# Optimization experiments

Hardware: AMD Instinct MI355X
Metric: run time of the kernel (lower is better)

## Reference

```python
import jax, jax.numpy as jnp
import numpy as np

GROUPS = 32
EPS = 1e-6


def group_norm(x, gamma, beta):
    # x: [b, c, h, w], normalize over (c//GROUPS, h, w) within each group
    b, c, h, w = x.shape
    xg = x.reshape(b, GROUPS, c // GROUPS, h, w)
    mu = xg.mean(axis=(2, 3, 4), keepdims=True)
    var = xg.var(axis=(2, 3, 4), keepdims=True)
    xn = ((xg - mu) * jax.lax.rsqrt(var + EPS)).reshape(b, c, h, w)
    return xn * gamma[None, :, None, None] + beta[None, :, None, None]


def conv1x1(x, W, b):
    # 1x1 conv == channel GEMM. W: [out_c, in_c]
    return jnp.einsum('bchw,oc->bohw', x, W) + b[None, :, None, None]


def setup_inputs() -> dict:
    key = jax.random.key(0)
    ks = jax.random.split(key, 4)
    B, C, H, W = 4, 512, 64, 64
    wscale = 0.02
    return {
        'x': jax.random.normal(ks[0], (B, C, H, W), dtype=jnp.float32),
        'gn_w': jnp.ones((C,), dtype=jnp.float32),
        'gn_b': jnp.zeros((C,), dtype=jnp.float32),
        'q_w': jax.random.normal(ks[1], (C, C), dtype=jnp.float32) * wscale,
        'q_b': jnp.zeros((C,), dtype=jnp.float32),
        'k_w': jax.random.normal(ks[2], (C, C), dtype=jnp.float32) * wscale,
        'k_b': jnp.zeros((C,), dtype=jnp.float32),
        'v_w': jax.random.normal(ks[3], (C, C), dtype=jnp.float32) * wscale,
        'v_b': jnp.zeros((C,), dtype=jnp.float32),
    }


def reference(x, gn_w, gn_b, q_w, q_b, k_w, k_b, v_w, v_b):
    h_ = group_norm(x, gn_w, gn_b)
    q = conv1x1(h_, q_w, q_b)
    k = conv1x1(h_, k_w, k_b)
    v = conv1x1(h_, v_w, v_b)
    b, c, h, w = q.shape
    hw = h * w
    qf = q.reshape(b, c, hw)
    kf = k.reshape(b, c, hw)
    vf = v.reshape(b, c, hw)
    # attn[b, i, j] = sum_c q[b, c, i] * k[b, c, j] / sqrt(c)
    attn = jnp.einsum('bci,bcj->bij', qf, kf) * (c ** -0.5)
    attn = jax.nn.softmax(attn, axis=2)
    # A[b, c, i] = sum_j v[b, c, j] * attn[b, i, j]  (== bmm(v, attn^T))
    A = jnp.einsum('bcj,bij->bci', vf, attn).reshape(b, c, h, w)
    return x + A
```

## Files before the change

kernel.cpp:

```cpp
#include <hip/hip_runtime.h>
#include <hip/hip_bf16.h>

typedef __hip_bfloat16 bf16;
typedef __attribute__((ext_vector_type(8))) short short8;
typedef __attribute__((ext_vector_type(4))) float f32x4;
typedef __attribute__((ext_vector_type(8))) unsigned short u16x8;
typedef __attribute__((ext_vector_type(4))) unsigned short u16x4;

#define HWSZ 4096
#define CH 512
#define BATCH 4
#define NGROUPS 32
#define CPG 16
#define PER ((size_t)CH * HWSZ)

#define GLL16(gp, lp)                                                         \
  __builtin_amdgcn_global_load_lds(                                           \
      (const __attribute__((address_space(1))) void*)(gp),                    \
      (__attribute__((address_space(3))) void*)(lp), 16, 0, 0)

__device__ __forceinline__ float b2f(bf16 v) { return __bfloat162float(v); }
__device__ __forceinline__ bf16 f2b(float v) { return __float2bfloat16(v); }

__global__ void gn_part_kernel(const float* __restrict__ x, float2* __restrict__ gpart) {
  int bg = blockIdx.x >> 3, chunk = blockIdx.x & 7;
  size_t base = (size_t)bg * (CPG * HWSZ) + (size_t)chunk * 8192;
  int tid = threadIdx.x;
  float s = 0.f, ss = 0.f;
  const float4* xp = (const float4*)(x + base);
#pragma unroll
  for (int it = 0; it < 8; ++it) {
    float4 v = xp[tid + it * 256];
    s += v.x + v.y + v.z + v.w;
    ss += v.x * v.x + v.y * v.y + v.z * v.z + v.w * v.w;
  }
  __shared__ float rs[256], rss[256];
  rs[tid] = s; rss[tid] = ss;
  __syncthreads();
  for (int off = 128; off > 0; off >>= 1) {
    if (tid < off) { rs[tid] += rs[tid + off]; rss[tid] += rss[tid + off]; }
    __syncthreads();
  }
  if (tid == 0) gpart[blockIdx.x] = make_float2(rs[0], rss[0]);
}

__global__ void gn_final_kernel(const float2* __restrict__ gpart,
                                const float* __restrict__ gw, const float* __restrict__ gb,
                                float* __restrict__ sca, float* __restrict__ shf) {
  int idx = blockIdx.x * 256 + threadIdx.x;
  int b = idx >> 9, c = idx & 511;
  int bg = b * NGROUPS + (c >> 4);
  float s = 0.f, ss = 0.f;
#pragma unroll
  for (int t = 0; t < 8; ++t) {
    float2 p = gpart[bg * 8 + t];
    s += p.x; ss += p.y;
  }
  const float N = (float)(CPG * HWSZ);
  float mu = s / N;
  float var = ss / N - mu * mu;
  float inv = rsqrtf(var + 1e-6f);
  float a = inv * gw[c];
  sca[idx] = a;
  shf[idx] = gb[c] - mu * a;
}

__global__ void wconv_kernel(const float* __restrict__ qw, const float* __restrict__ kw,
                             const float* __restrict__ vw,
                             bf16* __restrict__ wq, bf16* __restrict__ wk, bf16* __restrict__ wv) {
  int i = blockIdx.x * 256 + threadIdx.x;
  wq[i] = f2b(qw[i]);
  wk[i] = f2b(kw[i]);
  wv[i] = f2b(vw[i]);
}

__global__ void h_apply_kernel(const float* __restrict__ x, const float* __restrict__ sca,
                               const float* __restrict__ shf, bf16* __restrict__ hT, int b0) {
  int p0 = blockIdx.x * 64, c0 = blockIdx.y * 64;
  int b = b0 + blockIdx.z;
  bf16* hTb = hT + (size_t)blockIdx.z * PER;
  __shared__ bf16 lt[64][66];
  int t = threadIdx.x;
  int pp = (t & 15) * 4, ccb = t >> 4;
#pragma unroll
  for (int it = 0; it < 4; ++it) {
    int cc = ccb + it * 16;
    int c = c0 + cc;
    float a = sca[b * CH + c], s = shf[b * CH + c];
    const float4 xv = *(const float4*)(x + ((size_t)(b * CH + c)) * HWSZ + p0 + pp);
    lt[cc][pp] = f2b(a * xv.x + s);
    lt[cc][pp + 1] = f2b(a * xv.y + s);
    lt[cc][pp + 2] = f2b(a * xv.z + s);
    lt[cc][pp + 3] = f2b(a * xv.w + s);
  }
  __syncthreads();
  int cc = (t & 15) * 4;
#pragma unroll
  for (int it = 0; it < 4; ++it) {
    int pr = (t >> 4) + it * 16;
    u16x4 o;
#pragma unroll
    for (int j = 0; j < 4; ++j) o[j] = *(const unsigned short*)&lt[cc + j][pr];
    *(u16x4*)(hTb + (size_t)(p0 + pr) * CH + c0 + cc) = o;
  }
}


__device__ __forceinline__ void mm_step(const bf16* la, const bf16* lb,
                                        f32x4 acc[4][4], int wm, int wn,
                                        int quad, int tm) {
#pragma unroll
  for (int kk = 0; kk < 2; ++kk) {
    const int go = ((kk * 4 + quad) ^ (tm & 7)) * 8;
    short8 aF[4], bF[4];
#pragma unroll
    for (int mt = 0; mt < 4; ++mt) {
      aF[mt] = *(const short8*)(la + (wm + mt * 16 + tm) * 64 + go);
      bF[mt] = *(const short8*)(lb + (wn + mt * 16 + tm) * 64 + go);
    }
#pragma unroll
    for (int mt = 0; mt < 4; ++mt)
#pragma unroll
      for (int nt = 0; nt < 4; ++nt)
        acc[mt][nt] = __builtin_amdgcn_mfma_f32_16x16x32_bf16(aF[mt], bF[nt],
                                                              acc[mt][nt], 0, 0, 0);
  }
}

#define MFMA_VARS()                                   \
  int tid = threadIdx.x;                              \
  int l = tid & 63, w = tid >> 6;                     \
  int quad = l >> 4, tm = l & 15;                     \
  int wm = (w & 1) * 64, wn = (w >> 1) * 64;          \
  int rr = l >> 3;                                    \
  int swz = ((l & 7) ^ rr) * 8;                       \
  bf16* stbase = smem + w * 2048

#define MSTAGE(bufsel, koff)                          \
  do {                                                \
    bf16* _d = stbase + (bufsel) * 16384;             \
    GLL16(sA0 + (koff), _d);                          \
    GLL16(sA1 + (koff), _d + 512);                    \
    GLL16(sA2 + (koff), _d + 1024);                   \
    GLL16(sA3 + (koff), _d + 1536);                   \
    GLL16(sB0 + (koff), _d + 8192);                   \
    GLL16(sB1 + (koff), _d + 8704);                   \
    GLL16(sB2 + (koff), _d + 9216);                   \
    GLL16(sB3 + (koff), _d + 9728);                   \
  } while (0)

#define MKLOOP(NS)                                                       \
  do {                                                                   \
    MSTAGE(0, 0);                                                        \
    for (int _t = 0; _t < (NS); ++_t) {                                  \
      if (_t + 1 < (NS)) {                                               \
        MSTAGE((_t + 1) & 1, (_t + 1) * 64);                             \
        asm volatile("s_waitcnt vmcnt(8)" ::: "memory");                 \
      } else {                                                           \
        asm volatile("s_waitcnt vmcnt(0)" ::: "memory");                 \
      }                                                                  \
      __builtin_amdgcn_s_barrier();                                      \
      mm_step(smem + (_t & 1) * 16384, smem + (_t & 1) * 16384 + 8192,   \
              acc, wm, wn, quad, tm);                                    \
      __builtin_amdgcn_s_barrier();                                      \
    }                                                                    \
  } while (0)


#define MFMA_VARS256()                                \
  int tid = threadIdx.x;                              \
  int l = tid & 63, w = tid >> 6;                     \
  int quad = l >> 4, tm = l & 15;                     \
  int wm2 = (w & 1) * 128, wn2 = (w >> 1) * 64;       \
  int rr = l >> 3;                                    \
  int swz = ((l & 7) ^ rr) * 8

#define MSTAGE256(bufsel, koff)                        \
  do {                                                 \
    bf16* _d = smem + (bufsel) * 32768 + w * 2048;     \
    GLL16(sA0 + (koff), _d);                           \
    GLL16(sA1 + (koff), _d + 512);                     \
    GLL16(sA2 + (koff), _d + 1024);                    \
    GLL16(sA3 + (koff), _d + 1536);                    \
    GLL16(sB0 + (koff), _d + 16384);                   \
    GLL16(sB1 + (koff), _d + 16896);                   \
    GLL16(sB2 + (koff), _d + 17408);                   \
    GLL16(sB3 + (koff), _d + 17920);                   \
  } while (0)

#define MKLOOP256(NS)                                                          \
  do {                                                                         \
    MSTAGE256(0, 0);                                                           \
    asm volatile("s_waitcnt vmcnt(0)" ::: "memory");                           \
    __builtin_amdgcn_s_barrier();                                              \
    for (int _t = 0; _t < (NS); ++_t) {                                        \
      const bf16* lA = smem + (_t & 1) * 32768;                                \
      const bf16* lB = lA + 16384;                                             \
      short8 bF[4];                                                            \
      _Pragma("unroll")                                                        \
      for (int ph = 0; ph < 4; ++ph) {                                         \
        const int kk = ph >> 1, hh = ph & 1;                                   \
        if (ph == 0 && _t + 1 < (NS)) MSTAGE256((_t + 1) & 1, (_t + 1) * 64);  \
        if (hh == 0) {                                                         \
          _Pragma("unroll")                                                    \
          for (int nt = 0; nt < 4; ++nt) {                                     \
            int rb = wn2 + nt * 16 + tm;                                       \
            bF[nt] = *(const short8*)(lB + rb * 64 +                           \
                                      (((kk * 4 + quad) ^ (rb & 7)) * 8));     \
          }                                                                    \
        }                                                                      \
        short8 aF[4];                                                          \
        _Pragma("unroll")                                                      \
        for (int mt = 0; mt < 4; ++mt) {                                       \
          int ra = wm2 + hh * 64 + mt * 16 + tm;                               \
          aF[mt] = *(const short8*)(lA + ra * 64 +                             \
                                    (((kk * 4 + quad) ^ (ra & 7)) * 8));       \
        }                                                                      \
        __builtin_amdgcn_s_barrier();                                          \
        __builtin_amdgcn_s_setprio(1);                                         \
        _Pragma("unroll")                                                      \
        for (int mt = 0; mt < 4; ++mt)                                         \
          _Pragma("unroll")                                                    \
          for (int nt = 0; nt < 4; ++nt)                                       \
            acc[hh * 4 + mt][nt] = __builtin_amdgcn_mfma_f32_16x16x32_bf16(    \
                aF[mt], bF[nt], acc[hh * 4 + mt][nt], 0, 0, 0);                \
        __builtin_amdgcn_s_setprio(0);                                         \
        if (ph == 3 && _t + 1 < (NS))                                          \
          asm volatile("s_waitcnt vmcnt(0)" ::: "memory");                     \
        __builtin_amdgcn_s_barrier();                                          \
      }                                                                        \
    }                                                                          \
  } while (0)

__global__ __launch_bounds__(256) void qkv_mfma(const bf16* __restrict__ hT,
                                                const bf16* __restrict__ wq,
                                                const bf16* __restrict__ wk,
                                                const bf16* __restrict__ wv,
                                                const float* __restrict__ qb,
                                                const float* __restrict__ kb,
                                                const float* __restrict__ vb,
                                                bf16* __restrict__ qT, bf16* __restrict__ kT,
                                                bf16* __restrict__ v) {
  int p0 = blockIdx.x * 128;
  int o0 = blockIdx.y * 128;
  int bz = blockIdx.z / 3, z = blockIdx.z % 3;
  const bf16* W = z == 0 ? wq : (z == 1 ? wk : wv);
  const float* bias = z == 0 ? qb : (z == 1 ? kb : vb);
  const bf16* hTb = hT + (size_t)bz * PER;
  __shared__ __align__(16) bf16 smem[32768];
  MFMA_VARS();
  const bf16* sA0 = hTb + (size_t)(p0 + w * 32 + rr) * CH + swz;
  const bf16* sA1 = sA0 + (size_t)8 * CH;
  const bf16* sA2 = sA0 + (size_t)16 * CH;
  const bf16* sA3 = sA0 + (size_t)24 * CH;
  const bf16* sB0 = W + (size_t)(o0 + w * 32 + rr) * CH + swz;
  const bf16* sB1 = sB0 + (size_t)8 * CH;
  const bf16* sB2 = sB0 + (size_t)16 * CH;
  const bf16* sB3 = sB0 + (size_t)24 * CH;
  f32x4 acc[4][4] = {};
  MKLOOP(CH / 64);
  if (z < 2) {
    bf16* outT = (z == 0 ? qT : kT) + (size_t)bz * PER;
#pragma unroll
    for (int nt = 0; nt < 4; ++nt) {
      int o = o0 + wn + nt * 16 + tm;
      float bv = bias[o];
#pragma unroll
      for (int mt = 0; mt < 4; ++mt)
#pragma unroll
        for (int r = 0; r < 4; ++r) {
          int p = p0 + wm + mt * 16 + quad * 4 + r;
          outT[(size_t)p * CH + o] = f2b(acc[mt][nt][r] + bv);
        }
    }
  } else {
    bf16* vv = v + (size_t)bz * PER;
    bf16* lt = smem;
    for (int chunk = 0; chunk < 2; ++chunk) {
      __syncthreads();
      if (wn == chunk * 64) {
#pragma unroll
        for (int nt = 0; nt < 4; ++nt) {
          int o = o0 + wn + nt * 16 + tm;
          float bv = bias[o];
#pragma unroll
          for (int mt = 0; mt < 4; ++mt)
#pragma unroll
            for (int r = 0; r < 4; ++r)
              lt[(nt * 16 + tm) * 136 + wm + mt * 16 + quad * 4 + r] = f2b(acc[mt][nt][r] + bv);
        }
      }
      __syncthreads();
      int oo = tid >> 2, ppb = (tid & 3) * 32;
      bf16* dst = vv + (size_t)(o0 + chunk * 64 + oo) * HWSZ + p0 + ppb;
      const bf16* src = lt + oo * 136 + ppb;
#pragma unroll
      for (int q4 = 0; q4 < 4; ++q4)
        *(u16x8*)(dst + q4 * 8) = *(const u16x8*)(src + q4 * 8);
    }
  }
}

__global__ __launch_bounds__(512, 2) void s_mfma(const bf16* __restrict__ qT,
                                                 const bf16* __restrict__ kT,
                                                 bf16* __restrict__ attn,
                                                 float* __restrict__ lsum) {
  int j0 = blockIdx.x * 256;
  int il0 = blockIdx.y * 256;
  int bz = blockIdx.z;
  const bf16* qTb = qT + (size_t)bz * PER;
  const bf16* kTb = kT + (size_t)bz * PER;
  bf16* attnb = attn + (size_t)bz * HWSZ * HWSZ;
  float* lsumb = lsum + (size_t)bz * HWSZ;
  __shared__ __align__(16) bf16 smem[65536];
  MFMA_VARS256();
  const bf16* sA0 = qTb + (size_t)(il0 + w * 32 + rr) * CH + swz;
  const bf16* sA1 = sA0 + (size_t)8 * CH;
  const bf16* sA2 = sA0 + (size_t)16 * CH;
  const bf16* sA3 = sA0 + (size_t)24 * CH;
  const bf16* sB0 = kTb + (size_t)(j0 + w * 32 + rr) * CH + swz;
  const bf16* sB1 = sB0 + (size_t)8 * CH;
  const bf16* sB2 = sB0 + (size_t)16 * CH;
  const bf16* sB3 = sB0 + (size_t)24 * CH;
  f32x4 acc[8][4] = {};
  MKLOOP256(CH / 64);
  const float scale = 0.044194173824159216f;
#pragma unroll
  for (int m8 = 0; m8 < 8; ++m8)
#pragma unroll
    for (int r = 0; r < 4; ++r) {
      int il = il0 + wm2 + m8 * 16 + quad * 4 + r;
      float rs = 0.f;
#pragma unroll
      for (int nt = 0; nt < 4; ++nt) {
        float p = __expf(acc[m8][nt][r] * scale);
        rs += p;
        attnb[(size_t)il * HWSZ + j0 + wn2 + nt * 16 + tm] = f2b(p);
      }
      rs += __shfl_xor(rs, 1);
      rs += __shfl_xor(rs, 2);
      rs += __shfl_xor(rs, 4);
      rs += __shfl_xor(rs, 8);
      if (tm == 0) atomicAdd(&lsumb[il], rs);
    }
}

__global__ __launch_bounds__(512, 2) void a_mfma(const bf16* __restrict__ v,
                                                 const bf16* __restrict__ attn,
                                                 float* __restrict__ acc_out,
                                                 int KC, int ksplit) {
  int il0 = blockIdx.x * 256;
  int c00 = blockIdx.y * 256;
  int bz = blockIdx.z / ksplit;
  int kbase = (blockIdx.z % ksplit) * KC;
  const bf16* vb = v + (size_t)bz * PER;
  const bf16* attnb = attn + (size_t)bz * HWSZ * HWSZ;
  float* accb = acc_out + (size_t)bz * CH * HWSZ;
  __shared__ __align__(16) bf16 smem[65536];
  MFMA_VARS256();
  const bf16* sA0 = vb + (size_t)(c00 + w * 32 + rr) * HWSZ + kbase + swz;
  const bf16* sA1 = sA0 + (size_t)8 * HWSZ;
  const bf16* sA2 = sA0 + (size_t)16 * HWSZ;
  const bf16* sA3 = sA0 + (size_t)24 * HWSZ;
  const bf16* sB0 = attnb + (size_t)(il0 + w * 32 + rr) * HWSZ + kbase + swz;
  const bf16* sB1 = sB0 + (size_t)8 * HWSZ;
  const bf16* sB2 = sB0 + (size_t)16 * HWSZ;
  const bf16* sB3 = sB0 + (size_t)24 * HWSZ;
  f32x4 acc[8][4] = {};
  MKLOOP256(KC / 64);
#pragma unroll
  for (int m8 = 0; m8 < 8; ++m8)
#pragma unroll
    for (int nt = 0; nt < 4; ++nt)
#pragma unroll
      for (int r = 0; r < 4; ++r) {
        int c = c00 + wm2 + m8 * 16 + quad * 4 + r;
        int il = il0 + wn2 + nt * 16 + tm;
        atomicAdd(&accb[(size_t)c * HWSZ + il], acc[m8][nt][r]);
      }
}

__global__ void add_kernel(const float* __restrict__ x, const float* __restrict__ acc,
                           const float* __restrict__ lsum, float* __restrict__ out, int b0) {
  int idx = blockIdx.x * 256 + threadIdx.x;
  int b = b0 + blockIdx.y;
  const float* accb = acc + (size_t)blockIdx.y * CH * HWSZ;
  const float* lsumb = lsum + (size_t)blockIdx.y * HWSZ;
  int c = idx >> 10;
  int r4 = (idx & 1023) * 4;
  size_t g = ((size_t)(b * CH + c)) * HWSZ + r4;
  const float4 xv = *(const float4*)(x + g);
  const float4 av = *(const float4*)(accb + (size_t)c * HWSZ + r4);
  const float4 lv = *(const float4*)(lsumb + r4);
  float4 o;
  o.x = xv.x + av.x / lv.x;
  o.y = xv.y + av.y / lv.y;
  o.z = xv.z + av.z / lv.z;
  o.w = xv.w + av.w / lv.w;
  *(float4*)(out + g) = o;
}

extern "C" void kernel_launch(void* const* d_in, const int* in_sizes, int n_in,
                              void* d_out, int out_size, void* d_ws, size_t ws_size,
                              hipStream_t stream) {
  const float* x   = (const float*)d_in[0];
  const float* gnw = (const float*)d_in[1];
  const float* gnb = (const float*)d_in[2];
  const float* qw  = (const float*)d_in[3];
  const float* qb  = (const float*)d_in[4];
  const float* kw  = (const float*)d_in[5];
  const float* kb  = (const float*)d_in[6];
  const float* vw  = (const float*)d_in[7];
  const float* vb  = (const float*)d_in[8];
  float* out = (float*)d_out;

  char* ws = (char*)d_ws;
  float* sca = (float*)ws;
  float* shf = sca + BATCH * CH;
  float2* gpart = (float2*)(ws + 16384);
  const size_t wsz = (size_t)CH * CH;
  bf16* wqb = (bf16*)(ws + 32768);
  bf16* wkb = wqb + wsz;
  bf16* wvb = wkb + wsz;
  char* dyn = (char*)(wvb + wsz);
  size_t base_used = (size_t)(dyn - ws);
  size_t perb = 4 * PER * sizeof(bf16) + (size_t)HWSZ * HWSZ * sizeof(bf16) +
                (size_t)CH * HWSZ * sizeof(float) + (size_t)HWSZ * sizeof(float);
  int nb = (int)(((long long)ws_size - (long long)base_used) / (long long)perb);
  if (nb < 1) nb = 1;
  if (nb > BATCH) nb = BATCH;
  bf16* hT = (bf16*)dyn;
  bf16* qT = hT + (size_t)nb * PER;
  bf16* kT = qT + (size_t)nb * PER;
  bf16* v  = kT + (size_t)nb * PER;
  bf16* attn = v + (size_t)nb * PER;
  float* acc = (float*)(attn + (size_t)nb * HWSZ * HWSZ);
  float* lsum = acc + (size_t)nb * CH * HWSZ;

  gn_part_kernel<<<dim3(BATCH * NGROUPS * 8), 256, 0, stream>>>(x, gpart);
  gn_final_kernel<<<dim3(8), 256, 0, stream>>>(gpart, gnw, gnb, sca, shf);
  wconv_kernel<<<dim3(wsz / 256), 256, 0, stream>>>(qw, kw, vw, wqb, wkb, wvb);
  for (int b0 = 0; b0 < BATCH; b0 += nb) {
    int nbc = BATCH - b0 < nb ? BATCH - b0 : nb;
    h_apply_kernel<<<dim3(HWSZ / 64, CH / 64, nbc), 256, 0, stream>>>(x, sca, shf, hT, b0);
    qkv_mfma<<<dim3(HWSZ / 128, CH / 128, 3 * nbc), 256, 0, stream>>>(hT, wqb, wkb, wvb,
                                                                      qb, kb, vb, qT, kT, v);
    hipMemsetAsync(acc, 0, (size_t)nbc * CH * HWSZ * sizeof(float), stream);
    hipMemsetAsync(lsum, 0, (size_t)nbc * HWSZ * sizeof(float), stream);
    int ksplit = 256 / (16 * (CH / 256) * nbc);
    if (ksplit < 1) ksplit = 1;
    if (ksplit > 4) ksplit = 4;
    while (ksplit & (ksplit - 1)) --ksplit;
    int KC = HWSZ / ksplit;
    s_mfma<<<dim3(HWSZ / 256, HWSZ / 256, nbc), 512, 0, stream>>>(qT, kT, attn, lsum);
    a_mfma<<<dim3(HWSZ / 256, CH / 256, ksplit * nbc), 512, 0, stream>>>(v, attn, acc, KC, ksplit);
    add_kernel<<<dim3((CH * HWSZ) / 1024, nbc), 256, 0, stream>>>(x, acc, lsum, out, b0);
  }
}
```

Measured before the change: 367.6 us.

## Switch 256-tile GEMM mainloop to 4-stage, 32-wide K pipeline

```diff
diff --git a/kernel.cpp b/kernel.cpp
--- a/kernel.cpp
+++ b/kernel.cpp
@@ -172,49 +172,45 @@
   int l = tid & 63, w = tid >> 6;                     \
   int quad = l >> 4, tm = l & 15;                     \
   int wm2 = (w & 1) * 128, wn2 = (w >> 1) * 64;       \
-  int rr = l >> 3;                                    \
-  int swz = ((l & 7) ^ rr) * 8
+  int sr = l >> 2;                                    \
+  int swz = ((l & 3) ^ ((l >> 3) & 3)) * 8;           \
+  int go = (quad ^ ((tm >> 1) & 3)) * 8
 
 #define MSTAGE256(bufsel, koff)                        \
   do {                                                 \
-    bf16* _d = smem + (bufsel) * 32768 + w * 2048;     \
+    bf16* _d = smem + (bufsel) * 16384 + w * 1024;     \
     GLL16(sA0 + (koff), _d);                           \
     GLL16(sA1 + (koff), _d + 512);                     \
-    GLL16(sA2 + (koff), _d + 1024);                    \
-    GLL16(sA3 + (koff), _d + 1536);                    \
-    GLL16(sB0 + (koff), _d + 16384);                   \
-    GLL16(sB1 + (koff), _d + 16896);                   \
-    GLL16(sB2 + (koff), _d + 17408);                   \
-    GLL16(sB3 + (koff), _d + 17920);                   \
+    GLL16(sB0 + (koff), _d + 8192);                    \
+    GLL16(sB1 + (koff), _d + 8704);                    \
   } while (0)
 
 #define MKLOOP256(NS)                                                          \
   do {                                                                         \
     MSTAGE256(0, 0);                                                           \
-    asm volatile("s_waitcnt vmcnt(0)" ::: "memory");                           \
+    MSTAGE256(1, 32);                                                          \
+    MSTAGE256(2, 64);                                                          \
+    asm volatile("s_waitcnt vmcnt(8)" ::: "memory");        \
     __builtin_amdgcn_s_barrier();                                              \
     for (int _t = 0; _t < (NS); ++_t) {                                        \
-      const bf16* lA = smem + (_t & 1) * 32768;                                \
-      const bf16* lB = lA + 16384;                                             \
+      const bf16* lA = smem + (_t & 3) * 16384;                                \
+      const bf16* lB = lA + 8192;                                              \
       short8 bF[4];                                                            \
       _Pragma("unroll")                                                        \
-      for (int ph = 0; ph < 4; ++ph) {                                         \
-        const int kk = ph >> 1, hh = ph & 1;                                   \
-        if (ph == 0 && _t + 1 < (NS)) MSTAGE256((_t + 1) & 1, (_t + 1) * 64);  \
+      for (int hh = 0; hh < 2; ++hh) {                                         \
         if (hh == 0) {                                                         \
+          if (_t + 3 < (NS)) MSTAGE256((_t + 3) & 3, (_t + 3) * 32);           \
           _Pragma("unroll")                                                    \
           for (int nt = 0; nt < 4; ++nt) {                                     \
             int rb = wn2 + nt * 16 + tm;                                       \
-            bF[nt] = *(const short8*)(lB + rb * 64 +                           \
-                                      (((kk * 4 + quad) ^ (rb & 7)) * 8));     \
+            bF[nt] = *(const short8*)(lB + rb * 32 + go);                      \
           }                                                                    \
         }                                                                      \
         short8 aF[4];                                                          \
         _Pragma("unroll")                                                      \
         for (int mt = 0; mt < 4; ++mt) {                                       \
           int ra = wm2 + hh * 64 + mt * 16 + tm;                               \
-          aF[mt] = *(const short8*)(lA + ra * 64 +                             \
-                                    (((kk * 4 + quad) ^ (ra & 7)) * 8));       \
+          aF[mt] = *(const short8*)(lA + ra * 32 + go);                        \
         }                                                                      \
         __builtin_amdgcn_s_barrier();                                          \
         __builtin_amdgcn_s_setprio(1);                                         \
@@ -225,8 +221,14 @@
             acc[hh * 4 + mt][nt] = __builtin_amdgcn_mfma_f32_16x16x32_bf16(    \
                 aF[mt], bF[nt], acc[hh * 4 + mt][nt], 0, 0, 0);                \
         __builtin_amdgcn_s_setprio(0);                                         \
-        if (ph == 3 && _t + 1 < (NS))                                          \
-          asm volatile("s_waitcnt vmcnt(0)" ::: "memory");                     \
+        if (hh == 1) {                                                         \
+          if (_t + 3 < (NS))                                                   \
+            asm volatile("s_waitcnt vmcnt(8)" ::: "memory");                   \
+          else if (_t + 3 == (NS))                                             \
+            asm volatile("s_waitcnt vmcnt(4)" ::: "memory");                   \
+          else if (_t + 1 < (NS))                                              \
+            asm volatile("s_waitcnt vmcnt(0)" ::: "memory");                   \
+        }                                                                      \
         __builtin_amdgcn_s_barrier();                                          \
       }                                                                        \
     }                                                                          \
@@ -314,16 +316,12 @@
   float* lsumb = lsum + (size_t)bz * HWSZ;
   __shared__ __align__(16) bf16 smem[65536];
   MFMA_VARS256();
-  const bf16* sA0 = qTb + (size_t)(il0 + w * 32 + rr) * CH + swz;
-  const bf16* sA1 = sA0 + (size_t)8 * CH;
-  const bf16* sA2 = sA0 + (size_t)16 * CH;
-  const bf16* sA3 = sA0 + (size_t)24 * CH;
-  const bf16* sB0 = kTb + (size_t)(j0 + w * 32 + rr) * CH + swz;
-  const bf16* sB1 = sB0 + (size_t)8 * CH;
-  const bf16* sB2 = sB0 + (size_t)16 * CH;
-  const bf16* sB3 = sB0 + (size_t)24 * CH;
+  const bf16* sA0 = qTb + (size_t)(il0 + w * 32 + sr) * CH + swz;
+  const bf16* sA1 = sA0 + (size_t)16 * CH;
+  const bf16* sB0 = kTb + (size_t)(j0 + w * 32 + sr) * CH + swz;
+  const bf16* sB1 = sB0 + (size_t)16 * CH;
   f32x4 acc[8][4] = {};
-  MKLOOP256(CH / 64);
+  MKLOOP256(CH / 32);
   const float scale = 0.044194173824159216f;
 #pragma unroll
   for (int m8 = 0; m8 < 8; ++m8)
@@ -358,16 +356,12 @@
   float* accb = acc_out + (size_t)bz * CH * HWSZ;
   __shared__ __align__(16) bf16 smem[65536];
   MFMA_VARS256();
-  const bf16* sA0 = vb + (size_t)(c00 + w * 32 + rr) * HWSZ + kbase + swz;
-  const bf16* sA1 = sA0 + (size_t)8 * HWSZ;
-  const bf16* sA2 = sA0 + (size_t)16 * HWSZ;
-  const bf16* sA3 = sA0 + (size_t)24 * HWSZ;
-  const bf16* sB0 = attnb + (size_t)(il0 + w * 32 + rr) * HWSZ + kbase + swz;
-  const bf16* sB1 = sB0 + (size_t)8 * HWSZ;
-  const bf16* sB2 = sB0 + (size_t)16 * HWSZ;
-  const bf16* sB3 = sB0 + (size_t)24 * HWSZ;
+  const bf16* sA0 = vb + (size_t)(c00 + w * 32 + sr) * HWSZ + kbase + swz;
+  const bf16* sA1 = sA0 + (size_t)16 * HWSZ;
+  const bf16* sB0 = attnb + (size_t)(il0 + w * 32 + sr) * HWSZ + kbase + swz;
+  const bf16* sB1 = sB0 + (size_t)16 * HWSZ;
   f32x4 acc[8][4] = {};
-  MKLOOP256(KC / 64);
+  MKLOOP256(KC / 32);
 #pragma unroll
   for (int m8 = 0; m8 < 8; ++m8)
 #pragma unroll
```

New measurement: 372.8 us. About the same (+1.4%).
